# Kernel tuning notes

Hardware: AMD Instinct MI355X
Metric: run time of the kernel (lower is better)

The kernel has to match this reference:

```python
import jax, jax.numpy as jnp
import numpy as np

B, S, HID = 2, 1024, 1024
H, P, D = 16, 2, 64
SCALE = 1.0 / np.sqrt(D)


def setup_inputs() -> dict:
    key = jax.random.key(0)
    ks = jax.random.split(key, 9)
    hidden_states = jax.random.normal(ks[0], (B, S, HID), dtype=jnp.float32)
    w_std = 0.02
    Wq = jax.random.normal(ks[1], (HID, HID), dtype=jnp.float32) * w_std
    Wk = jax.random.normal(ks[2], (HID, HID), dtype=jnp.float32) * w_std
    Wv = jax.random.normal(ks[3], (HID, HID), dtype=jnp.float32) * w_std
    Wo = jax.random.normal(ks[4], (HID, HID), dtype=jnp.float32) * w_std
    # alpha_* initialized as identity over heads, broadcast over pseudo dim, plus noise
    ident = jnp.broadcast_to(jnp.eye(H, dtype=jnp.float32)[:, :, None], (H, H, P))
    alpha_q = ident + 0.01 * jax.random.normal(ks[5], (H, H, P), dtype=jnp.float32)
    alpha_k = ident + 0.01 * jax.random.normal(ks[6], (H, H, P), dtype=jnp.float32)
    alpha_v = ident + 0.01 * jax.random.normal(ks[7], (H, H, P), dtype=jnp.float32)
    # collapse: (H, H*P), one-hot picking pseudo-head 0 of each head, plus noise
    collapse = jnp.zeros((H, H * P), dtype=jnp.float32)
    hi = jnp.arange(H)
    collapse = collapse.at[hi, hi * P].set(1.0)
    collapse = collapse + 0.01 * jax.random.normal(ks[8], (H, H * P), dtype=jnp.float32)
    return {"hidden_states": hidden_states, "Wq": Wq, "Wk": Wk, "Wv": Wv, "Wo": Wo,
            "alpha_q": alpha_q, "alpha_k": alpha_k, "alpha_v": alpha_v, "collapse": collapse}


def _iha_forward(x, Wq, Wk, Wv, Wo, alpha_q, alpha_k, alpha_v, collapse):
    b, s, _ = x.shape
    # projections (torch F.linear: x @ W^T), split into heads -> (b, H, s, D)
    def proj(W):
        return jnp.einsum('bse,fe->bsf', x, W).reshape(b, s, H, D).transpose(0, 2, 1, 3)
    q, k, v = proj(Wq), proj(Wk), proj(Wv)
    # head mixing: mhp,bmnd->bhpnd then merge pseudo into virtual seq (b,H,s*P,D)
    def mix_merge(alpha, t):
        t = jnp.einsum('mhp,bmnd->bhpnd', alpha, t)
        return t.transpose(0, 1, 3, 2, 4).reshape(b, H, s * P, D)
    q, k, v = mix_merge(alpha_q, q), mix_merge(alpha_k, k), mix_merge(alpha_v, v)
    # causal SDPA over virtual positions
    sv = s * P
    scores = jnp.einsum('bhqd,bhkd->bhqk', q, k) * jnp.asarray(SCALE, x.dtype)
    vpos = jnp.arange(sv)
    causal = vpos[:, None] >= vpos[None, :]
    scores = jnp.where(causal, scores, jnp.asarray(-jnp.inf, x.dtype))
    probs = jax.nn.softmax(scores, axis=-1)
    attn = jnp.einsum('bhqk,bhkd->bhqd', probs, v)  # (b, H, sv, D)
    # collapse pseudo heads: (b,H,s,P,D) -> (b,s,H*P,D) -> einsum with collapse
    attn = attn.reshape(b, H, s, P, D).transpose(0, 2, 1, 3, 4).reshape(b, s, H * P, D)
    attn = jnp.einsum('ho,bnod->bhnd', collapse, attn)  # (b, H, s, D)
    attn = attn.transpose(0, 2, 1, 3).reshape(b, s, HID)
    return jnp.einsum('bse,fe->bsf', attn, Wo)


def reference(hidden_states, Wq, Wk, Wv, Wo, alpha_q, alpha_k, alpha_v, collapse):
    return _iha_forward(hidden_states, Wq, Wk, Wv, Wo, alpha_q, alpha_k, alpha_v, collapse)
```

## Files before the change

### kernel.cpp

```cpp
#include <hip/hip_runtime.h>
#include <hip/hip_bf16.h>

#define B_    2
#define S_    1024
#define HID_  1024
#define H_    16
#define P_    2
#define D_    64
#define SV_   2048
#define NBH_  32
#define SCALE_LOG2E 0.18033688f

typedef __attribute__((ext_vector_type(8))) short short8;
typedef __attribute__((ext_vector_type(4))) float f32x4;

#if __has_builtin(__builtin_amdgcn_exp2f)
#define EXP2(x) __builtin_amdgcn_exp2f(x)
#else
#define EXP2(x) exp2f(x)
#endif

__device__ __forceinline__ unsigned short f2bf(float f) {
  union { float f; unsigned u; } v; v.f = f;
  unsigned r = v.u + 0x7fffu + ((v.u >> 16) & 1u);
  return (unsigned short)(r >> 16);
}
__device__ __forceinline__ unsigned pack_bf2(float a, float b) {
  __hip_bfloat162 h = __float22bfloat162_rn(make_float2(a, b));
  unsigned u; __builtin_memcpy(&u, &h, 4);
  return u;
}

__global__ __launch_bounds__(256) void cast_f32_bf16(
    const float* __restrict__ src, unsigned short* __restrict__ dst, int n4) {
  int i = blockIdx.x * blockDim.x + threadIdx.x;
  int stride = gridDim.x * blockDim.x;
  for (; i < n4; i += stride) {
    float4 v = ((const float4*)src)[i];
    ushort4 o;
    o.x = f2bf(v.x); o.y = f2bf(v.y); o.z = f2bf(v.z); o.w = f2bf(v.w);
    ((ushort4*)dst)[i] = o;
  }
}

__global__ __launch_bounds__(256) void weff_kernel(
    const float* __restrict__ Wq, const float* __restrict__ Wk,
    const float* __restrict__ Wv,
    const float* __restrict__ aq, const float* __restrict__ ak,
    const float* __restrict__ av,
    unsigned short* __restrict__ Weff) {
  __shared__ float Al[16][32];
  const int d = blockIdx.x;
  const int t = blockIdx.y;
  const float* W = (t == 0) ? Wq : ((t == 1) ? Wk : Wv);
  const float* A = (t == 0) ? aq : ((t == 1) ? ak : av);
  const int tid = threadIdx.x;
  for (int idx = tid; idx < 512; idx += 256) Al[idx >> 5][idx & 31] = A[idx];
  __syncthreads();
  const int e = tid * 4;
  float wr[16][4];
#pragma unroll
  for (int m = 0; m < 16; ++m) {
    float4 v = *(const float4*)(W + (size_t)(m * 64 + d) * 1024 + e);
    wr[m][0] = v.x; wr[m][1] = v.y; wr[m][2] = v.z; wr[m][3] = v.w;
  }
  for (int hp = 0; hp < 32; ++hp) {
    float acc0 = 0.f, acc1 = 0.f, acc2 = 0.f, acc3 = 0.f;
#pragma unroll
    for (int m = 0; m < 16; ++m) {
      float al = Al[m][hp];
      acc0 += al * wr[m][0]; acc1 += al * wr[m][1];
      acc2 += al * wr[m][2]; acc3 += al * wr[m][3];
    }
    int r = (hp >> 1) * 128 + (hp & 1) * 64 + d;
    ushort4 ov;
    ov.x = f2bf(acc0); ov.y = f2bf(acc1); ov.z = f2bf(acc2); ov.w = f2bf(acc3);
    *(ushort4*)(Weff + ((size_t)t * 2048 + r) * 1024 + e) = ov;
  }
}

__global__ __launch_bounds__(256) void woeff_kernel(
    const float* __restrict__ Wo, const float* __restrict__ coll,
    unsigned short* __restrict__ Woeff) {
  __shared__ float wrow[1024];
  __shared__ float cl[512];
  const int f = blockIdx.x;
  const int tid = threadIdx.x;
  for (int idx = tid; idx < 512; idx += 256) cl[idx] = coll[idx];
  for (int idx = tid; idx < 1024; idx += 256) wrow[idx] = Wo[(size_t)f * 1024 + idx];
  __syncthreads();
  for (int idx = tid; idx < 2048; idx += 256) {
    int o = idx >> 6, d = idx & 63;
    float acc = 0.f;
#pragma unroll
    for (int h = 0; h < 16; ++h) acc += wrow[h * 64 + d] * cl[h * 32 + o];
    Woeff[(size_t)f * 2048 + idx] = f2bf(acc);
  }
}

template <int OUTMODE>
__global__ __launch_bounds__(256) void gemm_bt(
    const unsigned short* __restrict__ A,
    const unsigned short* __restrict__ Bbase,
    int M, int N, int K,
    unsigned short* __restrict__ Qd, unsigned short* __restrict__ Kd,
    unsigned short* __restrict__ Vd, float* __restrict__ Cf) {
  __shared__ unsigned short As[2][128 * 32];
  __shared__ unsigned short Bs[2][128 * 32];
  const int t = threadIdx.x;
  const int wave = t >> 6, lane = t & 63, lrow = lane & 15, quad = lane >> 4;
  const int wm = wave >> 1, wn = wave & 1;
  const int row0 = blockIdx.x * 128;
  const int col0 = blockIdx.y * 128;
  const unsigned short* Bp = Bbase;
  if (OUTMODE == 0) Bp += (size_t)blockIdx.z * 2048 * 1024;

  const int r16 = lane >> 2;
  const int gc = (lane & 3) * 8;

  auto stage = [&](int k0, int buf) {
#pragma unroll
    for (int j = 0; j < 2; ++j) {
      const int cc = wave * 2 + j;
      const unsigned short* ga = A + (size_t)(row0 + cc * 16 + r16) * K + k0 + gc;
      __builtin_amdgcn_global_load_lds(
          (const __attribute__((address_space(1))) unsigned int*)ga,
          (__attribute__((address_space(3))) unsigned int*)(&As[buf][cc * 512]), 16, 0, 0);
      const unsigned short* gb = Bp + (size_t)(col0 + cc * 16 + r16) * K + k0 + gc;
      __builtin_amdgcn_global_load_lds(
          (const __attribute__((address_space(1))) unsigned int*)gb,
          (__attribute__((address_space(3))) unsigned int*)(&Bs[buf][cc * 512]), 16, 0, 0);
    }
  };

  f32x4 acc[4][4];
#pragma unroll
  for (int mi = 0; mi < 4; ++mi)
#pragma unroll
    for (int ni = 0; ni < 4; ++ni) acc[mi][ni] = (f32x4){0.f, 0.f, 0.f, 0.f};

  const int niter = K >> 5;
  stage(0, 0);

  for (int it = 0; it < niter; ++it) {
    const int buf = it & 1;
    if (it + 1 < niter) {
      stage((it + 1) * 32, buf ^ 1);
      asm volatile("s_waitcnt vmcnt(4)" ::: "memory");
    } else {
      asm volatile("s_waitcnt vmcnt(0)" ::: "memory");
    }
    asm volatile("s_barrier" ::: "memory");

    short8 af[4], bfr[4];
#pragma unroll
    for (int mi = 0; mi < 4; ++mi)
      af[mi] = *(const short8*)(&As[buf][(wm * 64 + mi * 16 + lrow) * 32 + quad * 8]);
#pragma unroll
    for (int ni = 0; ni < 4; ++ni)
      bfr[ni] = *(const short8*)(&Bs[buf][(wn * 64 + ni * 16 + lrow) * 32 + quad * 8]);
#pragma unroll
    for (int mi = 0; mi < 4; ++mi)
#pragma unroll
      for (int ni = 0; ni < 4; ++ni)
        acc[mi][ni] = __builtin_amdgcn_mfma_f32_16x16x32_bf16(af[mi], bfr[ni],
                                                              acc[mi][ni], 0, 0, 0);

    asm volatile("s_barrier" ::: "memory");
  }

#pragma unroll
  for (int mi = 0; mi < 4; ++mi) {
#pragma unroll
    for (int ni = 0; ni < 4; ++ni) {
#pragma unroll
      for (int i = 0; i < 4; ++i) {
        int grow = row0 + wm * 64 + mi * 16 + quad * 4 + i;
        int gcol = col0 + wn * 64 + ni * 16 + lrow;
        float val = acc[mi][ni][i];
        if (OUTMODE == 0) {
          int b = grow >> 10, n = grow & 1023;
          int h = gcol >> 7, p = (gcol >> 6) & 1, d = gcol & 63;
          int z = blockIdx.z;
          if (z == 2) {
            Vd[((size_t)((b * 16 + h) * 64 + d)) * 2048 + (n * 2 + p)] = f2bf(val);
          } else {
            unsigned short* dst = (z == 0) ? Qd : Kd;
            dst[((size_t)((b * 16 + h) * 2048) + n * 2 + p) * 64 + d] = f2bf(val);
          }
        } else {
          Cf[(size_t)grow * N + gcol] = val;
        }
      }
    }
  }
}

__global__ __launch_bounds__(256, 2) void attn_kernel(
    const unsigned short* __restrict__ Qv, const unsigned short* __restrict__ Kv,
    const unsigned short* __restrict__ Vt, unsigned short* __restrict__ Aov) {
  __shared__ unsigned short Ks[2][4096];
  __shared__ unsigned short Vs[2][4096];
  __shared__ unsigned short Plds[4][2048];
  const int bh = blockIdx.x;
  const int yy = blockIdx.y;
  const int qwin = (yy < 8) ? yy : (23 - yy);
  const int t = threadIdx.x;
  const int w = t >> 6, lane = t & 63, lq = lane & 15, quad = lane >> 4;
  const int l3 = lq & 7;

  const unsigned short* Qh = Qv + (size_t)bh * SV_ * D_;
  const unsigned short* Kh = Kv + (size_t)bh * SV_ * D_;
  const unsigned short* Vh = Vt + (size_t)bh * D_ * SV_;

  const int q0 = qwin * 128 + w * 32;
  short8 bq[2][2];
#pragma unroll
  for (int g = 0; g < 2; ++g)
#pragma unroll
    for (int c = 0; c < 2; ++c)
      bq[g][c] = *(const short8*)(Qh + (size_t)(q0 + g * 16 + lq) * 64 + c * 32 + quad * 8);

  const int sg = (lane & 7) ^ ((lane >> 3) & 7);
  const int r0 = w * 8 + (lane >> 3);
  const unsigned short* Kg0 = Kh + r0 * 64 + sg * 8;
  const unsigned short* Vg0 = Vh + (size_t)r0 * SV_ + sg * 8;
  const int lds0 = w * 512;
  const int lds1 = 2048 + w * 512;

  auto stage = [&](int kt) {
    const int buf = kt & 1;
    const unsigned short* kg = Kg0 + kt * 4096;
    const unsigned short* vg = Vg0 + kt * 64;
    __builtin_amdgcn_global_load_lds(
        (const __attribute__((address_space(1))) unsigned int*)kg,
        (__attribute__((address_space(3))) unsigned int*)(&Ks[buf][lds0]), 16, 0, 0);
    __builtin_amdgcn_global_load_lds(
        (const __attribute__((address_space(1))) unsigned int*)(kg + 32 * 64),
        (__attribute__((address_space(3))) unsigned int*)(&Ks[buf][lds1]), 16, 0, 0);
    __builtin_amdgcn_global_load_lds(
        (const __attribute__((address_space(1))) unsigned int*)vg,
        (__attribute__((address_space(3))) unsigned int*)(&Vs[buf][lds0]), 16, 0, 0);
    __builtin_amdgcn_global_load_lds(
        (const __attribute__((address_space(1))) unsigned int*)(vg + (size_t)32 * SV_),
        (__attribute__((address_space(3))) unsigned int*)(&Vs[buf][lds1]), 16, 0, 0);
  };

  unsigned short* Pw = Plds[w];
  const int qrg0 = q0 + lq;
  const int qrg1 = q0 + 16 + lq;

  float lacc[2] = {0.f, 0.f};
  f32x4 o_acc[4][2];
#pragma unroll
  for (int nd = 0; nd < 4; ++nd)
#pragma unroll
    for (int g = 0; g < 2; ++g) o_acc[nd][g] = (f32x4){0.f, 0.f, 0.f, 0.f};

  const int nt = 2 * qwin + 2;
  stage(0);

  for (int kt = 0; kt < nt; ++kt) {
    const int buf = kt & 1;
    if (kt + 1 < nt) {
      stage(kt + 1);
      asm volatile("s_waitcnt vmcnt(4)" ::: "memory");
    } else {
      asm volatile("s_waitcnt vmcnt(0)" ::: "memory");
    }
    asm volatile("s_barrier" ::: "memory");

    const unsigned short* Kb = Ks[buf];
    short8 ka[4][2];
#pragma unroll
    for (int t4 = 0; t4 < 4; ++t4)
#pragma unroll
      for (int c = 0; c < 2; ++c)
        ka[t4][c] = *(const short8*)(Kb + (t4 * 16 + lq) * 64 + (((c * 4 + quad) ^ l3) * 8));

    f32x4 s[4][2];
#pragma unroll
    for (int t4 = 0; t4 < 4; ++t4)
#pragma unroll
      for (int g = 0; g < 2; ++g) {
        f32x4 z = (f32x4){0.f, 0.f, 0.f, 0.f};
        z = __builtin_amdgcn_mfma_f32_16x16x32_bf16(ka[t4][0], bq[g][0], z, 0, 0, 0);
        s[t4][g] = __builtin_amdgcn_mfma_f32_16x16x32_bf16(ka[t4][1], bq[g][1], z, 0, 0, 0);
      }

    const bool diag = (kt >= 2 * qwin);
    const int kc0 = kt * 64 + quad * 4;
#pragma unroll
    for (int g = 0; g < 2; ++g) {
      const int qr = (g == 0) ? qrg0 : qrg1;
      float rs = 0.f;
#pragma unroll
      for (int t4 = 0; t4 < 4; ++t4) {
        float p[4];
#pragma unroll
        for (int i = 0; i < 4; ++i) {
          float e = EXP2(s[t4][g][i] * SCALE_LOG2E);
          if (diag) e = (kc0 + t4 * 16 + i > qr) ? 0.f : e;
          p[i] = e;
          rs += e;
        }
        uint2 dw;
        dw.x = pack_bf2(p[0], p[1]);
        dw.y = pack_bf2(p[2], p[3]);
        const int row = g * 16 + lq;
        const int cg = t4 * 2 + (quad >> 1);
        *(uint2*)(Pw + row * 64 + ((cg ^ l3) * 8) + (quad & 1) * 4) = dw;
      }
      lacc[g] += rs;
    }

    const unsigned short* Vb = Vs[buf];
#pragma unroll
    for (int kh = 0; kh < 2; ++kh) {
      short8 va[4];
#pragma unroll
      for (int nd = 0; nd < 4; ++nd)
        va[nd] = *(const short8*)(Vb + (nd * 16 + lq) * 64 + (((kh * 4 + quad) ^ l3) * 8));
      short8 bp[2];
#pragma unroll
      for (int g = 0; g < 2; ++g)
        bp[g] = *(const short8*)(Pw + (g * 16 + lq) * 64 + (((kh * 4 + quad) ^ l3) * 8));
#pragma unroll
      for (int nd = 0; nd < 4; ++nd)
#pragma unroll
        for (int g = 0; g < 2; ++g)
          o_acc[nd][g] = __builtin_amdgcn_mfma_f32_16x16x32_bf16(va[nd], bp[g], o_acc[nd][g], 0, 0, 0);
    }

    asm volatile("s_barrier" ::: "memory");
  }

#pragma unroll
  for (int g = 0; g < 2; ++g) {
    lacc[g] += __shfl_xor(lacc[g], 16);
    lacc[g] += __shfl_xor(lacc[g], 32);
  }

  const int b = bh >> 4, h = bh & 15;
#pragma unroll
  for (int g = 0; g < 2; ++g) {
    const int qr = (g == 0) ? qrg0 : qrg1;
    const float inv = 1.0f / lacc[g];
    const int n = qr >> 1, p = qr & 1;
    unsigned short* dst = Aov + ((size_t)(b * 1024 + n)) * 2048 + (h * 2 + p) * 64;
#pragma unroll
    for (int nd = 0; nd < 4; ++nd) {
      uint2 dw;
      dw.x = pack_bf2(o_acc[nd][g][0] * inv, o_acc[nd][g][1] * inv);
      dw.y = pack_bf2(o_acc[nd][g][2] * inv, o_acc[nd][g][3] * inv);
      *(uint2*)(dst + nd * 16 + quad * 4) = dw;
    }
  }
}

extern "C" void kernel_launch(void* const* d_in, const int* in_sizes, int n_in,
                              void* d_out, int out_size, void* d_ws, size_t ws_size,
                              hipStream_t stream) {
  (void)in_sizes; (void)n_in; (void)out_size; (void)ws_size;
  const float* x    = (const float*)d_in[0];
  const float* Wq   = (const float*)d_in[1];
  const float* Wk   = (const float*)d_in[2];
  const float* Wv   = (const float*)d_in[3];
  const float* Wo   = (const float*)d_in[4];
  const float* aq   = (const float*)d_in[5];
  const float* ak   = (const float*)d_in[6];
  const float* av   = (const float*)d_in[7];
  const float* coll = (const float*)d_in[8];
  float* out = (float*)d_out;

  char* ws = (char*)d_ws;
  const size_t MB = 1024 * 1024;
  unsigned short* Xb    = (unsigned short*)(ws);
  unsigned short* Weff  = (unsigned short*)(ws + 6 * MB);
  unsigned short* Qv    = (unsigned short*)(ws + 18 * MB);
  unsigned short* Kv    = (unsigned short*)(ws + 26 * MB);
  unsigned short* Vt    = (unsigned short*)(ws + 34 * MB);
  unsigned short* Aov   = (unsigned short*)(ws + 6 * MB);
  unsigned short* Woeff = (unsigned short*)(ws + 14 * MB);

  cast_f32_bf16<<<dim3(1024), dim3(256), 0, stream>>>(x, Xb, (B_ * S_ * HID_) / 4);
  weff_kernel<<<dim3(64, 3), dim3(256), 0, stream>>>(Wq, Wk, Wv, aq, ak, av, Weff);
  gemm_bt<0><<<dim3(16, 16, 3), dim3(256), 0, stream>>>(
      Xb, Weff, 2048, 2048, 1024, Qv, Kv, Vt, nullptr);
  attn_kernel<<<dim3(32, 16), dim3(256), 0, stream>>>(Qv, Kv, Vt, Aov);
  woeff_kernel<<<dim3(1024), dim3(256), 0, stream>>>(Wo, coll, Woeff);
  gemm_bt<1><<<dim3(16, 8, 1), dim3(256), 0, stream>>>(
      Aov, Woeff, 2048, 1024, 2048, nullptr, nullptr, nullptr, out);
}
```

Baseline: 224.7 us.

## Retile attention to 64-query tiles, transpose V projection GEMM, narrow output GEMM tiles

The attention kernel now gives each wave 16 query rows instead of 32 and each block 64 queries instead of 128. The grid doubles to 1024 blocks, the occupancy hint rises to 4 blocks per CU, and the P scratch in LDS is halved. The V projection becomes a separate GEMM with swapped operands (Weff_v times X), so the transposed V store writes along the sequence dimension rather than with a large stride. The output projection uses a new 64x128-tile GEMM so that it launches more blocks. The aim is better CU utilisation and coalesced stores. The cost is an extra launch, less data reuse per block, and more register pressure from the higher occupancy target.

```diff
diff --git a/kernel.cpp b/kernel.cpp
--- a/kernel.cpp
+++ b/kernel.cpp
@@ -104,7 +104,7 @@
     const unsigned short* __restrict__ Bbase,
     int M, int N, int K,
     unsigned short* __restrict__ Qd, unsigned short* __restrict__ Kd,
-    unsigned short* __restrict__ Vd, float* __restrict__ Cf) {
+    unsigned short* __restrict__ Vd) {
   __shared__ unsigned short As[2][128 * 32];
   __shared__ unsigned short Bs[2][128 * 32];
   const int t = threadIdx.x;
@@ -112,6 +112,8 @@
   const int wm = wave >> 1, wn = wave & 1;
   const int row0 = blockIdx.x * 128;
   const int col0 = blockIdx.y * 128;
+  const unsigned short* Ap = A;
+  if (OUTMODE == 0) Ap += 0;
   const unsigned short* Bp = Bbase;
   if (OUTMODE == 0) Bp += (size_t)blockIdx.z * 2048 * 1024;
 
@@ -122,7 +124,7 @@
 #pragma unroll
     for (int j = 0; j < 2; ++j) {
       const int cc = wave * 2 + j;
-      const unsigned short* ga = A + (size_t)(row0 + cc * 16 + r16) * K + k0 + gc;
+      const unsigned short* ga = Ap + (size_t)(row0 + cc * 16 + r16) * K + k0 + gc;
       __builtin_amdgcn_global_load_lds(
           (const __attribute__((address_space(1))) unsigned int*)ga,
           (__attribute__((address_space(3))) unsigned int*)(&As[buf][cc * 512]), 16, 0, 0);
@@ -181,30 +183,104 @@
         if (OUTMODE == 0) {
           int b = grow >> 10, n = grow & 1023;
           int h = gcol >> 7, p = (gcol >> 6) & 1, d = gcol & 63;
-          int z = blockIdx.z;
-          if (z == 2) {
-            Vd[((size_t)((b * 16 + h) * 64 + d)) * 2048 + (n * 2 + p)] = f2bf(val);
-          } else {
-            unsigned short* dst = (z == 0) ? Qd : Kd;
-            dst[((size_t)((b * 16 + h) * 2048) + n * 2 + p) * 64 + d] = f2bf(val);
-          }
+          unsigned short* dst = (blockIdx.z == 0) ? Qd : Kd;
+          dst[((size_t)((b * 16 + h) * 2048) + n * 2 + p) * 64 + d] = f2bf(val);
         } else {
-          Cf[(size_t)grow * N + gcol] = val;
+          int h = grow >> 7, p = (grow >> 6) & 1, d = grow & 63;
+          int b = gcol >> 10, n = gcol & 1023;
+          Vd[((size_t)((b * 16 + h) * 64 + d)) * 2048 + n * 2 + p] = f2bf(val);
         }
       }
     }
   }
 }
 
-__global__ __launch_bounds__(256, 2) void attn_kernel(
+__global__ __launch_bounds__(256) void gemm64(
+    const unsigned short* __restrict__ A,
+    const unsigned short* __restrict__ Bbase,
+    int M, int N, int K, float* __restrict__ Cf) {
+  __shared__ unsigned short As[2][64 * 32];
+  __shared__ unsigned short Bs[2][128 * 32];
+  const int t = threadIdx.x;
+  const int wave = t >> 6, lane = t & 63, lrow = lane & 15, quad = lane >> 4;
+  const int row0 = blockIdx.x * 64;
+  const int col0 = blockIdx.y * 128;
+
+  const int r16 = lane >> 2;
+  const int gc = (lane & 3) * 8;
+
+  auto stage = [&](int k0, int buf) {
+    const unsigned short* ga = A + (size_t)(row0 + wave * 16 + r16) * K + k0 + gc;
+    __builtin_amdgcn_global_load_lds(
+        (const __attribute__((address_space(1))) unsigned int*)ga,
+        (__attribute__((address_space(3))) unsigned int*)(&As[buf][wave * 512]), 16, 0, 0);
+#pragma unroll
+    for (int j = 0; j < 2; ++j) {
+      const int cc = wave * 2 + j;
+      const unsigned short* gb = Bbase + (size_t)(col0 + cc * 16 + r16) * K + k0 + gc;
+      __builtin_amdgcn_global_load_lds(
+          (const __attribute__((address_space(1))) unsigned int*)gb,
+          (__attribute__((address_space(3))) unsigned int*)(&Bs[buf][cc * 512]), 16, 0, 0);
+    }
+  };
+
+  f32x4 acc[4][2];
+#pragma unroll
+  for (int mi = 0; mi < 4; ++mi)
+#pragma unroll
+    for (int ni = 0; ni < 2; ++ni) acc[mi][ni] = (f32x4){0.f, 0.f, 0.f, 0.f};
+
+  const int niter = K >> 5;
+  stage(0, 0);
+
+  for (int it = 0; it < niter; ++it) {
+    const int buf = it & 1;
+    if (it + 1 < niter) {
+      stage((it + 1) * 32, buf ^ 1);
+      asm volatile("s_waitcnt vmcnt(3)" ::: "memory");
+    } else {
+      asm volatile("s_waitcnt vmcnt(0)" ::: "memory");
+    }
+    asm volatile("s_barrier" ::: "memory");
+
+    short8 af[4], bfr[2];
+#pragma unroll
+    for (int mi = 0; mi < 4; ++mi)
+      af[mi] = *(const short8*)(&As[buf][(mi * 16 + lrow) * 32 + quad * 8]);
+#pragma unroll
+    for (int ni = 0; ni < 2; ++ni)
+      bfr[ni] = *(const short8*)(&Bs[buf][(wave * 32 + ni * 16 + lrow) * 32 + quad * 8]);
+#pragma unroll
+    for (int mi = 0; mi < 4; ++mi)
+#pragma unroll
+      for (int ni = 0; ni < 2; ++ni)
+        acc[mi][ni] = __builtin_amdgcn_mfma_f32_16x16x32_bf16(af[mi], bfr[ni],
+                                                              acc[mi][ni], 0, 0, 0);
+
+    asm volatile("s_barrier" ::: "memory");
+  }
+
+#pragma unroll
+  for (int mi = 0; mi < 4; ++mi)
+#pragma unroll
+    for (int ni = 0; ni < 2; ++ni)
+#pragma unroll
+      for (int i = 0; i < 4; ++i) {
+        int grow = row0 + mi * 16 + quad * 4 + i;
+        int gcol = col0 + wave * 32 + ni * 16 + lrow;
+        Cf[(size_t)grow * N + gcol] = acc[mi][ni][i];
+      }
+}
+
+__global__ __launch_bounds__(256, 4) void attn_kernel(
     const unsigned short* __restrict__ Qv, const unsigned short* __restrict__ Kv,
     const unsigned short* __restrict__ Vt, unsigned short* __restrict__ Aov) {
   __shared__ unsigned short Ks[2][4096];
   __shared__ unsigned short Vs[2][4096];
-  __shared__ unsigned short Plds[4][2048];
+  __shared__ unsigned short Plds[4][1024];
   const int bh = blockIdx.x;
   const int yy = blockIdx.y;
-  const int qwin = (yy < 8) ? yy : (23 - yy);
+  const int qt = (yy < 16) ? yy : (47 - yy);
   const int t = threadIdx.x;
   const int w = t >> 6, lane = t & 63, lq = lane & 15, quad = lane >> 4;
   const int l3 = lq & 7;
@@ -213,20 +289,16 @@
   const unsigned short* Kh = Kv + (size_t)bh * SV_ * D_;
   const unsigned short* Vh = Vt + (size_t)bh * D_ * SV_;
 
-  const int q0 = qwin * 128 + w * 32;
-  short8 bq[2][2];
-#pragma unroll
-  for (int g = 0; g < 2; ++g)
-#pragma unroll
-    for (int c = 0; c < 2; ++c)
-      bq[g][c] = *(const short8*)(Qh + (size_t)(q0 + g * 16 + lq) * 64 + c * 32 + quad * 8);
+  const int qrow = qt * 64 + w * 16 + lq;
+  short8 bq0 = *(const short8*)(Qh + (size_t)qrow * 64 + quad * 8);
+  short8 bq1 = *(const short8*)(Qh + (size_t)qrow * 64 + 32 + quad * 8);
 
   const int sg = (lane & 7) ^ ((lane >> 3) & 7);
-  const int r0 = w * 8 + (lane >> 3);
+  const int r0 = w * 16 + (lane >> 3);
   const unsigned short* Kg0 = Kh + r0 * 64 + sg * 8;
   const unsigned short* Vg0 = Vh + (size_t)r0 * SV_ + sg * 8;
-  const int lds0 = w * 512;
-  const int lds1 = 2048 + w * 512;
+  const int lds0 = w * 1024;
+  const int lds1 = lds0 + 512;
 
   auto stage = [&](int kt) {
     const int buf = kt & 1;
@@ -236,28 +308,24 @@
         (const __attribute__((address_space(1))) unsigned int*)kg,
         (__attribute__((address_space(3))) unsigned int*)(&Ks[buf][lds0]), 16, 0, 0);
     __builtin_amdgcn_global_load_lds(
-        (const __attribute__((address_space(1))) unsigned int*)(kg + 32 * 64),
+        (const __attribute__((address_space(1))) unsigned int*)(kg + 8 * 64),
         (__attribute__((address_space(3))) unsigned int*)(&Ks[buf][lds1]), 16, 0, 0);
     __builtin_amdgcn_global_load_lds(
         (const __attribute__((address_space(1))) unsigned int*)vg,
         (__attribute__((address_space(3))) unsigned int*)(&Vs[buf][lds0]), 16, 0, 0);
     __builtin_amdgcn_global_load_lds(
-        (const __attribute__((address_space(1))) unsigned int*)(vg + (size_t)32 * SV_),
+        (const __attribute__((address_space(1))) unsigned int*)(vg + (size_t)8 * SV_),
         (__attribute__((address_space(3))) unsigned int*)(&Vs[buf][lds1]), 16, 0, 0);
   };
 
   unsigned short* Pw = Plds[w];
-  const int qrg0 = q0 + lq;
-  const int qrg1 = q0 + 16 + lq;
-
-  float lacc[2] = {0.f, 0.f};
-  f32x4 o_acc[4][2];
-#pragma unroll
-  for (int nd = 0; nd < 4; ++nd)
-#pragma unroll
-    for (int g = 0; g < 2; ++g) o_acc[nd][g] = (f32x4){0.f, 0.f, 0.f, 0.f};
-
-  const int nt = 2 * qwin + 2;
+
+  float l_sum = 0.f;
+  f32x4 o_acc[4];
+#pragma unroll
+  for (int nd = 0; nd < 4; ++nd) o_acc[nd] = (f32x4){0.f, 0.f, 0.f, 0.f};
+
+  const int nt = qt + 1;
   stage(0);
 
   for (int kt = 0; kt < nt; ++kt) {
@@ -278,83 +346,62 @@
       for (int c = 0; c < 2; ++c)
         ka[t4][c] = *(const short8*)(Kb + (t4 * 16 + lq) * 64 + (((c * 4 + quad) ^ l3) * 8));
 
-    f32x4 s[4][2];
-#pragma unroll
-    for (int t4 = 0; t4 < 4; ++t4)
-#pragma unroll
-      for (int g = 0; g < 2; ++g) {
-        f32x4 z = (f32x4){0.f, 0.f, 0.f, 0.f};
-        z = __builtin_amdgcn_mfma_f32_16x16x32_bf16(ka[t4][0], bq[g][0], z, 0, 0, 0);
-        s[t4][g] = __builtin_amdgcn_mfma_f32_16x16x32_bf16(ka[t4][1], bq[g][1], z, 0, 0, 0);
+    f32x4 s[4];
+#pragma unroll
+    for (int t4 = 0; t4 < 4; ++t4) {
+      f32x4 z = (f32x4){0.f, 0.f, 0.f, 0.f};
+      z = __builtin_amdgcn_mfma_f32_16x16x32_bf16(ka[t4][0], bq0, z, 0, 0, 0);
+      s[t4] = __builtin_amdgcn_mfma_f32_16x16x32_bf16(ka[t4][1], bq1, s[t4] = z, 0, 0, 0);
+    }
+
+    const bool diag = (kt == qt);
+    const int kc0 = kt * 64 + quad * 4;
+    float rs = 0.f;
+#pragma unroll
+    for (int t4 = 0; t4 < 4; ++t4) {
+      float p[4];
+#pragma unroll
+      for (int i = 0; i < 4; ++i) {
+        float e = EXP2(s[t4][i] * SCALE_LOG2E);
+        if (diag) e = (kc0 + t4 * 16 + i > qrow) ? 0.f : e;
+        p[i] = e;
+        rs += e;
       }
-
-    const bool diag = (kt >= 2 * qwin);
-    const int kc0 = kt * 64 + quad * 4;
-#pragma unroll
-    for (int g = 0; g < 2; ++g) {
-      const int qr = (g == 0) ? qrg0 : qrg1;
-      float rs = 0.f;
-#pragma unroll
-      for (int t4 = 0; t4 < 4; ++t4) {
-        float p[4];
-#pragma unroll
-        for (int i = 0; i < 4; ++i) {
-          float e = EXP2(s[t4][g][i] * SCALE_LOG2E);
-          if (diag) e = (kc0 + t4 * 16 + i > qr) ? 0.f : e;
-          p[i] = e;
-          rs += e;
-        }
-        uint2 dw;
-        dw.x = pack_bf2(p[0], p[1]);
-        dw.y = pack_bf2(p[2], p[3]);
-        const int row = g * 16 + lq;
-        const int cg = t4 * 2 + (quad >> 1);
-        *(uint2*)(Pw + row * 64 + ((cg ^ l3) * 8) + (quad & 1) * 4) = dw;
+      uint2 dw;
+      dw.x = pack_bf2(p[0], p[1]);
+      dw.y = pack_bf2(p[2], p[3]);
+      const int cg = t4 * 2 + (quad >> 1);
+      *(uint2*)(Pw + lq * 64 + ((cg ^ l3) * 8) + (quad & 1) * 4) = dw;
+    }
+    l_sum += rs;
+
+    const unsigned short* Vb = Vs[buf];
+#pragma unroll
+    for (int kh = 0; kh < 2; ++kh) {
+      short8 bp = *(const short8*)(Pw + lq * 64 + (((kh * 4 + quad) ^ l3) * 8));
+#pragma unroll
+      for (int nd = 0; nd < 4; ++nd) {
+        short8 va = *(const short8*)(Vb + (nd * 16 + lq) * 64 + (((kh * 4 + quad) ^ l3) * 8));
+        o_acc[nd] = __builtin_amdgcn_mfma_f32_16x16x32_bf16(va, bp, o_acc[nd], 0, 0, 0);
       }
-      lacc[g] += rs;
-    }
-
-    const unsigned short* Vb = Vs[buf];
-#pragma unroll
-    for (int kh = 0; kh < 2; ++kh) {
-      short8 va[4];
-#pragma unroll
-      for (int nd = 0; nd < 4; ++nd)
-        va[nd] = *(const short8*)(Vb + (nd * 16 + lq) * 64 + (((kh * 4 + quad) ^ l3) * 8));
-      short8 bp[2];
-#pragma unroll
-      for (int g = 0; g < 2; ++g)
-        bp[g] = *(const short8*)(Pw + (g * 16 + lq) * 64 + (((kh * 4 + quad) ^ l3) * 8));
-#pragma unroll
-      for (int nd = 0; nd < 4; ++nd)
-#pragma unroll
-        for (int g = 0; g < 2; ++g)
-          o_acc[nd][g] = __builtin_amdgcn_mfma_f32_16x16x32_bf16(va[nd], bp[g], o_acc[nd][g], 0, 0, 0);
-    }
-
-    asm volatile("s_barrier" ::: "memory");
-  }
-
-#pragma unroll
-  for (int g = 0; g < 2; ++g) {
-    lacc[g] += __shfl_xor(lacc[g], 16);
-    lacc[g] += __shfl_xor(lacc[g], 32);
-  }
+    }
+
+    asm volatile("s_barrier" ::: "memory");
+  }
+
+  l_sum += __shfl_xor(l_sum, 16);
+  l_sum += __shfl_xor(l_sum, 32);
 
   const int b = bh >> 4, h = bh & 15;
-#pragma unroll
-  for (int g = 0; g < 2; ++g) {
-    const int qr = (g == 0) ? qrg0 : qrg1;
-    const float inv = 1.0f / lacc[g];
-    const int n = qr >> 1, p = qr & 1;
-    unsigned short* dst = Aov + ((size_t)(b * 1024 + n)) * 2048 + (h * 2 + p) * 64;
-#pragma unroll
-    for (int nd = 0; nd < 4; ++nd) {
-      uint2 dw;
-      dw.x = pack_bf2(o_acc[nd][g][0] * inv, o_acc[nd][g][1] * inv);
-      dw.y = pack_bf2(o_acc[nd][g][2] * inv, o_acc[nd][g][3] * inv);
-      *(uint2*)(dst + nd * 16 + quad * 4) = dw;
-    }
+  const float inv = 1.0f / l_sum;
+  const int n = qrow >> 1, p = qrow & 1;
+  unsigned short* dst = Aov + ((size_t)(b * 1024 + n)) * 2048 + (h * 2 + p) * 64;
+#pragma unroll
+  for (int nd = 0; nd < 4; ++nd) {
+    uint2 dw;
+    dw.x = pack_bf2(o_acc[nd][0] * inv, o_acc[nd][1] * inv);
+    dw.y = pack_bf2(o_acc[nd][2] * inv, o_acc[nd][3] * inv);
+    *(uint2*)(dst + nd * 16 + quad * 4) = dw;
   }
 }
 
@@ -385,10 +432,12 @@
 
   cast_f32_bf16<<<dim3(1024), dim3(256), 0, stream>>>(x, Xb, (B_ * S_ * HID_) / 4);
   weff_kernel<<<dim3(64, 3), dim3(256), 0, stream>>>(Wq, Wk, Wv, aq, ak, av, Weff);
-  gemm_bt<0><<<dim3(16, 16, 3), dim3(256), 0, stream>>>(
-      Xb, Weff, 2048, 2048, 1024, Qv, Kv, Vt, nullptr);
-  attn_kernel<<<dim3(32, 16), dim3(256), 0, stream>>>(Qv, Kv, Vt, Aov);
+  gemm_bt<0><<<dim3(16, 16, 2), dim3(256), 0, stream>>>(
+      Xb, Weff, 2048, 2048, 1024, Qv, Kv, nullptr);
+  gemm_bt<2><<<dim3(16, 16), dim3(256), 0, stream>>>(
+      Weff + (size_t)2 * 2048 * 1024, Xb, 2048, 2048, 1024, nullptr, nullptr, Vt);
+  attn_kernel<<<dim3(32, 32), dim3(256), 0, stream>>>(Qv, Kv, Vt, Aov);
   woeff_kernel<<<dim3(1024), dim3(256), 0, stream>>>(Wo, coll, Woeff);
-  gemm_bt<1><<<dim3(16, 8, 1), dim3(256), 0, stream>>>(
-      Aov, Woeff, 2048, 1024, 2048, nullptr, nullptr, nullptr, out);
-}
+  gemm64<<<dim3(32, 8), dim3(256), 0, stream>>>(
+      Aov, Woeff, 2048, 1024, 2048, out);
+}
```

Result: faster. 216.2 us (-3.8%).
